# Optimization experiments

Measured on AMD Instinct MI355X. Metric: run time of the kernel, lower is better.

## Reference

```python
import jax, jax.numpy as jnp
import numpy as np

ALPHA = 0.2   # LeakyReLU negative slope
NEG = -9e15   # mask fill value from the torch code


def _conv1d(x, w, b):
    # x: (N, C_in, L), w: (C_out, C_in, 5), padding=2 -> same length
    y = jax.lax.conv_general_dilated(x, w, window_strides=(1,), padding=[(2, 2)],
                                     dimension_numbers=('NCH', 'OIH', 'NCH'))
    return y + b[None, :, None]


def _gat(h, mask, W, a):
    # Faithful to a_input @ a: e_ij = leakyrelu(Wh_i . a[:H] + Wh_j . a[H:])
    Wh = jnp.einsum('bnf,fo->bno', h, W)          # (B,N,H)
    H = W.shape[1]
    f1 = Wh @ a[:H]                               # (B,N,1)
    f2 = Wh @ a[H:]                               # (B,N,1)
    e = f1 + jnp.swapaxes(f2, 1, 2)               # (B,N,N)
    e = jnp.where(e > 0, e, ALPHA * e)            # LeakyReLU
    e = jnp.where(mask, e, NEG)
    att = jax.nn.softmax(e, axis=-1)              # dropout skipped (eval mode)
    return jnp.einsum('bij,bjo->bio', att, Wh)


def setup_inputs() -> dict:
    key = jax.random.key(0)
    ks = jax.random.split(key, 14)
    B, S, N, H, E = 8, 200, 512, 64, 2048
    sc = 0.1
    return {
        'x': jax.random.normal(ks[0], (B, S, N * 2), dtype=jnp.float32),
        'adj': jax.random.randint(ks[1], (N, N), 0, 2, dtype=jnp.int32),
        'edge_index': jax.random.randint(ks[2], (E, 2), 0, N, dtype=jnp.int32),
        'conv1_w': jax.random.normal(ks[3], (H // 2, 2, 5), dtype=jnp.float32) * sc,
        'conv1_b': jnp.zeros((H // 2,), dtype=jnp.float32),
        'conv2_w': jax.random.normal(ks[4], (H, H // 2, 5), dtype=jnp.float32) * sc,
        'conv2_b': jnp.zeros((H,), dtype=jnp.float32),
        'W1': jax.random.normal(ks[5], (H, H), dtype=jnp.float32) * sc,
        'a1': jax.random.normal(ks[6], (2 * H, 1), dtype=jnp.float32) * sc,
        'W2': jax.random.normal(ks[7], (H, H), dtype=jnp.float32) * sc,
        'a2': jax.random.normal(ks[8], (2 * H, 1), dtype=jnp.float32) * sc,
        'fc1_w': jax.random.normal(ks[9], (2 * H, H), dtype=jnp.float32) * sc,
        'fc1_b': jnp.zeros((H,), dtype=jnp.float32),
        'fc2_w': jax.random.normal(ks[10], (H, 1), dtype=jnp.float32) * sc,
        'fc2_b': jnp.zeros((1,), dtype=jnp.float32),
    }


def reference(x, adj, edge_index, conv1_w, conv1_b, conv2_w, conv2_b,
              W1, a1, W2, a2, fc1_w, fc1_b, fc2_w, fc2_b):
    B = x.shape[0]
    N = adj.shape[0]
    # (B,S,2N) -> (B,N,S,2) -> (B*N,2,S)
    xn = x.reshape(B, -1, N, 2).transpose(0, 2, 1, 3)
    xf = xn.reshape(B * N, -1, 2).transpose(0, 2, 1)
    h = jax.nn.relu(_conv1d(xf, conv1_w, conv1_b))
    h = jax.nn.relu(_conv1d(h, conv2_w, conv2_b))
    h = h.mean(axis=-1)                 # AdaptiveAvgPool1d(1) + squeeze
    h = h.reshape(B, N, -1)             # (B,N,H)
    mask = (adj > 0)[None]              # (1,N,N) broadcasts over batch
    h = jax.nn.relu(_gat(h, mask, W1, a1))
    h = _gat(h, mask, W2, a2)
    h1 = h[:, edge_index[:, 0]]         # (B,E,H)
    h2 = h[:, edge_index[:, 1]]
    he = jnp.concatenate([h1, h2], axis=-1)  # (B,E,2H)
    z = jax.nn.relu(he @ fc1_w + fc1_b)
    return jax.nn.sigmoid(z @ fc2_w + fc2_b).squeeze(-1)  # (B,E)
```

## Files before the change

kernel.cpp:

```cpp
#include <hip/hip_runtime.h>
#include <hip/hip_bf16.h>

typedef unsigned short u16;
typedef __attribute__((ext_vector_type(8))) short short8;
typedef __attribute__((ext_vector_type(4))) float float4v;

#define BATCH 8
#define SLEN  200
#define NNODE 512
#define NEDGE 2048
#define NEGV  -9000000000000000.0f

#define H1S 40
#define H1R 212

__device__ __forceinline__ u16 f2bf(float f) {
    unsigned int x = __float_as_uint(f);
    unsigned int lsb = (x >> 16) & 1u;
    x += 0x7fffu + lsb;
    return (u16)(x >> 16);
}

__device__ __forceinline__ float bf2f(u16 u) {
    return __uint_as_float(((unsigned int)u) << 16);
}

__device__ __forceinline__ unsigned int pk2(float a, float b) {
    __hip_bfloat162 h = __float22bfloat162_rn(make_float2(a, b));
    unsigned int r;
    __builtin_memcpy(&r, &h, 4);
    return r;
}

__global__ __launch_bounds__(256) void pre_kernel(
    const int* __restrict__ adj,
    const float* __restrict__ w2,
    const float* __restrict__ fc1w,
    const float* __restrict__ W2g,
    u16* __restrict__ w2f,
    u16* __restrict__ efw,
    u16* __restrict__ w2gf,
    u16* __restrict__ msk)
{
    const int t = threadIdx.x;
    const int blk = blockIdx.x;

    if (blk == 0) {
        for (int idx = t; idx < 20 * 64 * 8; idx += 256) {
            const int fid = idx >> 9, rem = idx & 511;
            const int lane = rem >> 3, j = rem & 7;
            const int kk = fid >> 2, ot = fid & 3;
            const int ml = lane & 15, q = lane >> 4;
            const int c  = q * 8 + j;
            const int ic = (c & 1) * 16 + (c >> 1);
            const int oc = ot * 16 + ml;
            w2f[idx] = f2bf(w2[(size_t)oc * 160 + ic * 5 + kk]);
        }
        return;
    }
    if (blk == 1) {
        for (int idx = t; idx < 16 * 64 * 8; idx += 256) {
            const int u = idx >> 9, rem = idx & 511;
            const int lane = rem >> 3, j = rem & 7;
            const int ks = u >> 2, wvv = u & 3;
            const int ml = lane & 15, q = lane >> 4;
            const int o = wvv * 16 + ml;
            const int k = ks * 32 + q * 8 + j;
            efw[idx] = f2bf(fc1w[k * 64 + o]);
        }
        return;
    }
    if (blk == 2) {
        for (int idx = t; idx < 8 * 64 * 8; idx += 256) {
            const int u = idx >> 9, rem = idx & 511;
            const int lane = rem >> 3, j = rem & 7;
            const int kh = u >> 2, nt = u & 3;
            const int ml = lane & 15, q = lane >> 4;
            const int o = nt * 16 + ml;
            const int k = kh * 32 + q * 8 + j;
            w2gf[idx] = f2bf(W2g[k * 64 + o]);
        }
        return;
    }

    {
        const int tid   = (blk - 3) * 256 + t;
        const int row   = tid >> 5;
        const int chunk = tid & 31;
        const int4* ap = (const int4*)(adj + (size_t)row * 512 + chunk * 16);
        const int4 a0 = ap[0], a1 = ap[1], a2 = ap[2], a3 = ap[3];
        unsigned int bits = 0;
        bits |= (a0.x > 0) ? 0x0001u : 0u;  bits |= (a0.y > 0) ? 0x0002u : 0u;
        bits |= (a0.z > 0) ? 0x0004u : 0u;  bits |= (a0.w > 0) ? 0x0008u : 0u;
        bits |= (a1.x > 0) ? 0x0010u : 0u;  bits |= (a1.y > 0) ? 0x0020u : 0u;
        bits |= (a1.z > 0) ? 0x0040u : 0u;  bits |= (a1.w > 0) ? 0x0080u : 0u;
        bits |= (a2.x > 0) ? 0x0100u : 0u;  bits |= (a2.y > 0) ? 0x0200u : 0u;
        bits |= (a2.z > 0) ? 0x0400u : 0u;  bits |= (a2.w > 0) ? 0x0800u : 0u;
        bits |= (a3.x > 0) ? 0x1000u : 0u;  bits |= (a3.y > 0) ? 0x2000u : 0u;
        bits |= (a3.z > 0) ? 0x4000u : 0u;  bits |= (a3.w > 0) ? 0x8000u : 0u;
        msk[row * 32 + chunk] = (u16)bits;
    }
}

__global__ __launch_bounds__(256) void conv_fused_kernel(
    const float* __restrict__ x,
    const float* __restrict__ w1,
    const float* __restrict__ b1,
    const float* __restrict__ b2,
    const float* __restrict__ W1,
    const float* __restrict__ a1,
    const u16* __restrict__ w2f,
    u16* __restrict__ Wh_bt,
    float* __restrict__ f1,
    float* __restrict__ f2)
{
    __shared__ float xs[2][2][212];
    __shared__ __align__(16) u16 h1p[H1R * H1S];
    __shared__ float red[4][2][32];
    __shared__ float hm[2][64];
    __shared__ float part[2][4][64];

    const int t    = threadIdx.x;
    const int blk  = blockIdx.x;
    const int b    = blk >> 8;
    const int pair = blk & 255;
    const int n0   = pair * 2;
    const int lane = t & 63;
    const int wv   = t >> 6;
    const int ml   = lane & 15;
    const int q    = lane >> 4;
    const int p = t & 15;
    const int g = t >> 4;
    const int o2 = wv & 1;
    const int mh = wv >> 1;

    short8 wfA[5], wfB[5];
    #pragma unroll
    for (int kk = 0; kk < 5; ++kk) {
        wfA[kk] = *(const short8*)(w2f + ((kk * 4 + o2 * 2 + 0) * 64 + lane) * 8);
        wfB[kk] = *(const short8*)(w2f + ((kk * 4 + o2 * 2 + 1) * 64 + lane) * 8);
    }
    const float bias2a = b2[o2 * 32 + ml];
    const float bias2b = b2[o2 * 32 + 16 + ml];

    float wA[10], wB[10];
    #pragma unroll
    for (int j = 0; j < 10; ++j) {
        wA[j] = w1[p * 10 + j];
        wB[j] = w1[(16 + p) * 10 + j];
    }
    const float b1a = b1[p], b1b = b1[16 + p];

    if (t < SLEN) {
        const float4 xv = *(const float4*)(x + ((size_t)(b * SLEN + t)) * 1024 + 4 * pair);
        xs[0][0][2 + t] = xv.x;
        xs[0][1][2 + t] = xv.y;
        xs[1][0][2 + t] = xv.z;
        xs[1][1][2 + t] = xv.w;
    } else if (t < 212) {
        const int pp = (t < 202) ? (t - 200) : t;
        xs[0][0][pp] = 0.f; xs[0][1][pp] = 0.f;
        xs[1][0][pp] = 0.f; xs[1][1][pp] = 0.f;
    }
    {
        unsigned int* hz = (unsigned int*)h1p;
        if (t < 40)       hz[t] = 0u;
        else if (t < 240) hz[4000 + t] = 0u;
    }
    __syncthreads();

    float tAn[2], tBn[2];
    for (int nd = 0; nd < 2; ++nd) {
        #pragma unroll
        for (int u = 0; u < 4; ++u) {
            const int base = 4 * g + 64 * u;
            if (base < SLEN) {
                float X0[8], X1[8];
                *(float4*)&X0[0] = *(const float4*)&xs[nd][0][base];
                *(float4*)&X0[4] = *(const float4*)&xs[nd][0][base + 4];
                *(float4*)&X1[0] = *(const float4*)&xs[nd][1][base];
                *(float4*)&X1[4] = *(const float4*)&xs[nd][1][base + 4];
                #pragma unroll
                for (int i = 0; i < 4; ++i) {
                    float a0 = b1a, a1v = b1b;
                    #pragma unroll
                    for (int k = 0; k < 5; ++k) {
                        const float x0 = X0[i + k], x1 = X1[i + k];
                        a0  += wA[k] * x0 + wA[5 + k] * x1;
                        a1v += wB[k] * x0 + wB[5 + k] * x1;
                    }
                    *(unsigned int*)&h1p[(2 + base + i) * H1S + 2 * p] =
                        pk2(fmaxf(a0, 0.f), fmaxf(a1v, 0.f));
                }
            }
        }
        __syncthreads();

        float tA = 0.f, tB = 0.f;
        const int mt0 = mh * 7, mtE = mh ? 13 : 7;
        for (int mt = mt0; mt < mtE; ++mt) {
            float4v acc0 = {0.f, 0.f, 0.f, 0.f};
            float4v acc1 = {0.f, 0.f, 0.f, 0.f};
            #pragma unroll
            for (int kk = 0; kk < 5; ++kk) {
                const short8 a = *(const short8*)&h1p[(mt * 16 + ml + kk) * H1S + q * 8];
                acc0 = __builtin_amdgcn_mfma_f32_16x16x32_bf16(a, wfA[kk], acc0, 0, 0, 0);
                acc1 = __builtin_amdgcn_mfma_f32_16x16x32_bf16(a, wfB[kk], acc1, 0, 0, 0);
            }
            if (mt < 12) {
                #pragma unroll
                for (int r = 0; r < 4; ++r) {
                    tA += fmaxf(acc0[r] + bias2a, 0.f);
                    tB += fmaxf(acc1[r] + bias2b, 0.f);
                }
            } else if (q < 2) {
                #pragma unroll
                for (int r = 0; r < 4; ++r) {
                    tA += fmaxf(acc0[r] + bias2a, 0.f);
                    tB += fmaxf(acc1[r] + bias2b, 0.f);
                }
            }
        }
        tA += __shfl_xor(tA, 16, 64);
        tA += __shfl_xor(tA, 32, 64);
        tB += __shfl_xor(tB, 16, 64);
        tB += __shfl_xor(tB, 32, 64);
        tAn[nd] = tA;
        tBn[nd] = tB;
        __syncthreads();
    }

    if (lane < 16) {
        red[wv][0][ml]      = tAn[0];
        red[wv][0][16 + ml] = tBn[0];
        red[wv][1][ml]      = tAn[1];
        red[wv][1][16 + ml] = tBn[1];
    }
    __syncthreads();
    if (t < 128) {
        const int nd = t >> 6, o = t & 63;
        const int grp = (o >> 5), idx = o & 31;
        hm[nd][o] = (red[grp][nd][idx] + red[grp + 2][nd][idx]) * (1.0f / 200.0f);
    }
    __syncthreads();

    {
        const int o = t & 63, q4 = t >> 6;
        const float* Wp = W1 + (q4 * 16) * 64 + o;
        float p0 = 0.f, p1 = 0.f;
        #pragma unroll
        for (int k = 0; k < 16; ++k) {
            const float w = Wp[k * 64];
            p0 += hm[0][q4 * 16 + k] * w;
            p1 += hm[1][q4 * 16 + k] * w;
        }
        part[0][q4][o] = p0;
        part[1][q4][o] = p1;
    }
    __syncthreads();
    if (t < 128) {
        const int nd = t >> 6, o = t & 63;
        const int n = n0 + nd;
        const float v = part[nd][0][o] + part[nd][1][o] + part[nd][2][o] + part[nd][3][o];
        Wh_bt[((size_t)(b * 64 + o)) * 512 + n] = f2bf(v);
        float v1 = v * a1[o];
        float v2 = v * a1[64 + o];
        #pragma unroll
        for (int off = 32; off; off >>= 1) {
            v1 += __shfl_xor(v1, off, 64);
            v2 += __shfl_xor(v2, off, 64);
        }
        if (o == 0) { f1[b * 512 + n] = v1; f2[b * 512 + n] = v2; }
    }
}

#define PSTR 520
__global__ __launch_bounds__(512) void gat_attn_kernel(
    const u16* __restrict__ Wh_bt,
    const float* __restrict__ f1in,
    const float* __restrict__ f2in,
    const u16* __restrict__ msk,
    const u16* __restrict__ w2gf,
    const float* __restrict__ a2,
    u16* __restrict__ whbt_out,
    float* __restrict__ f1out,
    float* __restrict__ f2out,
    float* __restrict__ outp,
    const int fuse)
{
    __shared__ __align__(16) u16 P[16 * PSTR];
    __shared__ float f2s[512];
    __shared__ float invs[16];
    __shared__ float f1s[16];
    __shared__ float accH[4][64][4];
    __shared__ __align__(16) u16 g1s[16 * 72];
    __shared__ __align__(16) u16 wh2s[64 * 20];
    __shared__ float fp1[4][16], fp2[4][16];

    const int t   = threadIdx.x;
    const int blk = blockIdx.x;
    const int b   = blk >> 5;
    const int i0  = (blk & 31) * 16;
    const int lane = t & 63, wv = t >> 6, nt = wv & 3, kh = wv >> 2;
    const int ml = lane & 15, q = lane >> 4;

    const u16* Bp = Wh_bt + ((size_t)(b * 64 + nt * 16 + ml)) * 512 + kh * 256 + q * 8;
    short8 bfr[8];
    #pragma unroll
    for (int ks = 0; ks < 8; ++ks)
        bfr[ks] = *(const short8*)(Bp + ks * 32);

    f2s[t & 511] = f2in[b * 512 + (t & 511)];
    if (t < 16) f1s[t] = f1in[b * 512 + i0 + t];
    __syncthreads();

    {
        const int i = t >> 5, jseg = t & 31;
        const float f1i = f1s[i];
        const unsigned int mbits = msk[(size_t)(i0 + i) * 32 + jseg];
        const float* f2p = f2s + jseg * 16;
        float ev[16];
        float mx = -3.0e38f;
        #pragma unroll
        for (int v = 0; v < 16; ++v) {
            float e = f1i + f2p[v];
            e = e > 0.f ? e : 0.2f * e;
            e = ((mbits >> v) & 1u) ? e : NEGV;
            ev[v] = e;
            mx = fmaxf(mx, e);
        }
        mx = fmaxf(mx, __shfl_xor(mx, 1, 64));
        mx = fmaxf(mx, __shfl_xor(mx, 2, 64));
        mx = fmaxf(mx, __shfl_xor(mx, 4, 64));
        mx = fmaxf(mx, __shfl_xor(mx, 8, 64));
        mx = fmaxf(mx, __shfl_xor(mx, 16, 64));
        float sum = 0.f;
        #pragma unroll
        for (int v = 0; v < 16; ++v) {
            const float ex = __expf(ev[v] - mx);
            ev[v] = ex;
            sum += ex;
        }
        sum += __shfl_xor(sum, 1, 64);
        sum += __shfl_xor(sum, 2, 64);
        sum += __shfl_xor(sum, 4, 64);
        sum += __shfl_xor(sum, 8, 64);
        sum += __shfl_xor(sum, 16, 64);
        if (jseg == 0) invs[i] = 1.0f / sum;
        unsigned int* prow = (unsigned int*)&P[i * PSTR + jseg * 16];
        #pragma unroll
        for (int v = 0; v < 8; ++v)
            prow[v] = pk2(ev[2 * v], ev[2 * v + 1]);
    }
    __syncthreads();

    float4v acc = {0.f, 0.f, 0.f, 0.f};
    #pragma unroll
    for (int ks = 0; ks < 8; ++ks) {
        const short8 afr = *(const short8*)&P[ml * PSTR + kh * 256 + ks * 32 + q * 8];
        acc = __builtin_amdgcn_mfma_f32_16x16x32_bf16(afr, bfr[ks], acc, 0, 0, 0);
    }
    if (kh == 1) {
        #pragma unroll
        for (int r = 0; r < 4; ++r) accH[nt][lane][r] = acc[r];
    }
    __syncthreads();
    if (kh == 0) {
        #pragma unroll
        for (int r = 0; r < 4; ++r) {
            const int i2 = q * 4 + r;
            float val = (acc[r] + accH[nt][lane][r]) * invs[i2];
            if (fuse) {
                val = fmaxf(val, 0.f);
                g1s[i2 * 72 + nt * 16 + ml] = f2bf(val);
            } else {
                outp[((size_t)(b * 512 + i0 + i2)) * 64 + nt * 16 + ml] = val;
            }
        }
    }

    if (!fuse) return;

    __syncthreads();
    const short8 af2 = *(const short8*)&g1s[ml * 72 + kh * 32 + q * 8];
    const short8 bf2v = *(const short8*)(w2gf + ((kh * 4 + nt) * 64 + lane) * 8);
    float4v c2 = {0.f, 0.f, 0.f, 0.f};
    c2 = __builtin_amdgcn_mfma_f32_16x16x32_bf16(af2, bf2v, c2, 0, 0, 0);
    if (kh == 1) {
        #pragma unroll
        for (int r = 0; r < 4; ++r) accH[nt][lane][r] = c2[r];
    }
    __syncthreads();
    if (kh == 0) {
        const int o = nt * 16 + ml;
        const float a2o1 = a2[o], a2o2 = a2[64 + o];
        #pragma unroll
        for (int r = 0; r < 4; ++r) {
            const float wv2 = c2[r] + accH[nt][lane][r];
            wh2s[o * 20 + q * 4 + r] = f2bf(wv2);
            float p1 = wv2 * a2o1, p2 = wv2 * a2o2;
            p1 += __shfl_xor(p1, 1, 64); p2 += __shfl_xor(p2, 1, 64);
            p1 += __shfl_xor(p1, 2, 64); p2 += __shfl_xor(p2, 2, 64);
            p1 += __shfl_xor(p1, 4, 64); p2 += __shfl_xor(p2, 4, 64);
            p1 += __shfl_xor(p1, 8, 64); p2 += __shfl_xor(p2, 8, 64);
            if (ml == 0) {
                fp1[nt][q * 4 + r] = p1;
                fp2[nt][q * 4 + r] = p2;
            }
        }
    }
    __syncthreads();
    if (t < 256) {
        const int o = t >> 2, seg = t & 3;
        *(uint2*)&whbt_out[((size_t)(b * 64 + o)) * 512 + i0 + seg * 4] =
            *(const uint2*)&wh2s[o * 20 + seg * 4];
    }
    if (t < 16) {
        f1out[b * 512 + i0 + t] = fp1[0][t] + fp1[1][t] + fp1[2][t] + fp1[3][t];
        f2out[b * 512 + i0 + t] = fp2[0][t] + fp2[1][t] + fp2[2][t] + fp2[3][t];
    }
}

#define FSTR 136
__global__ __launch_bounds__(256) void edge_mlp_kernel(
    const float* __restrict__ hg,
    const int* __restrict__ eidx,
    const u16* __restrict__ efw,
    const float* __restrict__ fc1b,
    const float* __restrict__ fc2w,
    const float* __restrict__ fc2b,
    float* __restrict__ out)
{
    __shared__ __align__(16) u16 he[16 * FSTR];
    __shared__ float part[16][4];

    const int t   = threadIdx.x;
    const int blk = blockIdx.x;
    const int b   = blk >> 7;
    const int e0  = (blk & 127) * 16;
    const int lane = t & 63, wv = t >> 6, ml = lane & 15, q = lane >> 4;

    short8 bw[4];
    #pragma unroll
    for (int ks = 0; ks < 4; ++ks)
        bw[ks] = *(const short8*)(efw + ((ks * 4 + wv) * 64 + lane) * 8);
    const int o = 16 * wv + ml;
    const float bo = fc1b[o];
    const float wo = fc2w[o];

    {
        const int ep = t >> 4, p = t & 15;
        const int e = e0 + ep;
        const int node = (p < 8) ? eidx[e * 2] : eidx[e * 2 + 1];
        const int c0 = (p & 7) * 8;
        const float* hp = hg + ((size_t)(b * 512 + node)) * 64 + c0;
        const float4 fa = *(const float4*)hp;
        const float4 fb = *(const float4*)(hp + 4);
        unsigned int* dst = (unsigned int*)&he[ep * FSTR + ((p < 8) ? 0 : 64) + c0];
        dst[0] = pk2(fa.x, fa.y);
        dst[1] = pk2(fa.z, fa.w);
        dst[2] = pk2(fb.x, fb.y);
        dst[3] = pk2(fb.z, fb.w);
    }
    __syncthreads();

    float4v acc = {0.f, 0.f, 0.f, 0.f};
    #pragma unroll
    for (int ks = 0; ks < 4; ++ks) {
        const short8 afr = *(const short8*)&he[ml * FSTR + ks * 32 + q * 8];
        acc = __builtin_amdgcn_mfma_f32_16x16x32_bf16(afr, bw[ks], acc, 0, 0, 0);
    }
    #pragma unroll
    for (int r = 0; r < 4; ++r) {
        float z = fmaxf(acc[r] + bo, 0.f) * wo;
        z += __shfl_xor(z, 1, 64);
        z += __shfl_xor(z, 2, 64);
        z += __shfl_xor(z, 4, 64);
        z += __shfl_xor(z, 8, 64);
        if (ml == 0) part[q * 4 + r][wv] = z;
    }
    __syncthreads();
    if (t < 16) {
        const float v = part[t][0] + part[t][1] + part[t][2] + part[t][3] + fc2b[0];
        out[b * 2048 + e0 + t] = 1.0f / (1.0f + __expf(-v));
    }
}

extern "C" void kernel_launch(void* const* d_in, const int* in_sizes, int n_in,
                              void* d_out, int out_size, void* d_ws, size_t ws_size,
                              hipStream_t stream) {
    const float* x    = (const float*)d_in[0];
    const int* adj    = (const int*)d_in[1];
    const int* eidx   = (const int*)d_in[2];
    const float* w1   = (const float*)d_in[3];
    const float* b1   = (const float*)d_in[4];
    const float* w2   = (const float*)d_in[5];
    const float* b2   = (const float*)d_in[6];
    const float* W1   = (const float*)d_in[7];
    const float* a1   = (const float*)d_in[8];
    const float* W2   = (const float*)d_in[9];
    const float* a2   = (const float*)d_in[10];
    const float* fc1w = (const float*)d_in[11];
    const float* fc1b = (const float*)d_in[12];
    const float* fc2w = (const float*)d_in[13];
    const float* fc2b = (const float*)d_in[14];
    float* out = (float*)d_out;

    float* ws = (float*)d_ws;
    const size_t R = (size_t)BATCH * NNODE;
    float* g     = ws;
    float* f1a   = g + R * 64;
    float* f2a   = f1a + R;
    float* f1b   = f2a + R;
    float* f2b   = f1b + R;
    u16*   whbt1 = (u16*)(f2b + R);
    u16*   whbt2 = whbt1 + R * 64;
    u16*   w2f   = whbt2 + R * 64;
    u16*   efw   = w2f + 10240;
    u16*   w2gf  = efw + 8192;
    u16*   msk   = w2gf + 4096;

    pre_kernel<<<dim3(67), dim3(256), 0, stream>>>(
        adj, w2, fc1w, W2, w2f, efw, w2gf, msk);
    conv_fused_kernel<<<dim3(2048), dim3(256), 0, stream>>>(
        x, w1, b1, b2, W1, a1, w2f, whbt1, f1a, f2a);
    gat_attn_kernel<<<dim3(256), dim3(512), 0, stream>>>(
        whbt1, f1a, f2a, msk, w2gf, a2, whbt2, f1b, f2b, g, 1);
    gat_attn_kernel<<<dim3(256), dim3(512), 0, stream>>>(
        whbt2, f1b, f2b, msk, w2gf, a2, whbt2, f1b, f2b, g, 0);
    edge_mlp_kernel<<<dim3(1024), dim3(256), 0, stream>>>(
        g, eidx, efw, fc1b, fc2w, fc2b, out);
}
```

Baseline: 135.1 us.

## Split fused conv kernel into conv1 and conv2 kernels via global bf16 buffer

```diff
diff --git a/kernel.cpp b/kernel.cpp
--- a/kernel.cpp
+++ b/kernel.cpp
@@ -11,8 +11,8 @@
 #define NEDGE 2048
 #define NEGV  -9000000000000000.0f
 
-#define H1S 40
-#define H1R 212
+#define H1GR 212
+#define H1GS 32
 
 __device__ __forceinline__ u16 f2bf(float f) {
     unsigned int x = __float_as_uint(f);
@@ -102,46 +102,21 @@
     }
 }
 
-__global__ __launch_bounds__(256) void conv_fused_kernel(
+__global__ __launch_bounds__(256) void conv1_kernel(
     const float* __restrict__ x,
     const float* __restrict__ w1,
     const float* __restrict__ b1,
-    const float* __restrict__ b2,
-    const float* __restrict__ W1,
-    const float* __restrict__ a1,
-    const u16* __restrict__ w2f,
-    u16* __restrict__ Wh_bt,
-    float* __restrict__ f1,
-    float* __restrict__ f2)
+    u16* __restrict__ h1g)
 {
     __shared__ float xs[2][2][212];
-    __shared__ __align__(16) u16 h1p[H1R * H1S];
-    __shared__ float red[4][2][32];
-    __shared__ float hm[2][64];
-    __shared__ float part[2][4][64];
 
     const int t    = threadIdx.x;
     const int blk  = blockIdx.x;
     const int b    = blk >> 8;
     const int pair = blk & 255;
-    const int n0   = pair * 2;
-    const int lane = t & 63;
-    const int wv   = t >> 6;
-    const int ml   = lane & 15;
-    const int q    = lane >> 4;
     const int p = t & 15;
     const int g = t >> 4;
-    const int o2 = wv & 1;
-    const int mh = wv >> 1;
-
-    short8 wfA[5], wfB[5];
-    #pragma unroll
-    for (int kk = 0; kk < 5; ++kk) {
-        wfA[kk] = *(const short8*)(w2f + ((kk * 4 + o2 * 2 + 0) * 64 + lane) * 8);
-        wfB[kk] = *(const short8*)(w2f + ((kk * 4 + o2 * 2 + 1) * 64 + lane) * 8);
-    }
-    const float bias2a = b2[o2 * 32 + ml];
-    const float bias2b = b2[o2 * 32 + 16 + ml];
+    const int ng0 = b * 512 + pair * 2;
 
     float wA[10], wB[10];
     #pragma unroll
@@ -162,15 +137,22 @@
         xs[0][0][pp] = 0.f; xs[0][1][pp] = 0.f;
         xs[1][0][pp] = 0.f; xs[1][1][pp] = 0.f;
     }
+
     {
-        unsigned int* hz = (unsigned int*)h1p;
-        if (t < 40)       hz[t] = 0u;
-        else if (t < 240) hz[4000 + t] = 0u;
-    }
-    __syncthreads();
-
-    float tAn[2], tBn[2];
+        unsigned int* hg32 = (unsigned int*)h1g;
+        for (int idx = t; idx < 384; idx += 256) {
+            const int nd = (idx >= 192);
+            const int i2 = idx - nd * 192;
+            const int off = (i2 < 32) ? i2 : (202 * 16 + (i2 - 32));
+            hg32[(size_t)(ng0 + nd) * (H1GR * 16) + off] = 0u;
+        }
+    }
+    __syncthreads();
+
+    unsigned int* hg32 = (unsigned int*)h1g;
+    #pragma unroll
     for (int nd = 0; nd < 2; ++nd) {
+        const size_t nbase = (size_t)(ng0 + nd) * (H1GR * 16);
         #pragma unroll
         for (int u = 0; u < 4; ++u) {
             const int base = 4 * g + 64 * u;
@@ -189,88 +171,110 @@
                         a0  += wA[k] * x0 + wA[5 + k] * x1;
                         a1v += wB[k] * x0 + wB[5 + k] * x1;
                     }
-                    *(unsigned int*)&h1p[(2 + base + i) * H1S + 2 * p] =
+                    hg32[nbase + (2 + base + i) * 16 + p] =
                         pk2(fmaxf(a0, 0.f), fmaxf(a1v, 0.f));
                 }
             }
         }
-        __syncthreads();
-
-        float tA = 0.f, tB = 0.f;
-        const int mt0 = mh * 7, mtE = mh ? 13 : 7;
-        for (int mt = mt0; mt < mtE; ++mt) {
-            float4v acc0 = {0.f, 0.f, 0.f, 0.f};
-            float4v acc1 = {0.f, 0.f, 0.f, 0.f};
+    }
+}
+
+__global__ __launch_bounds__(256) void conv2_kernel(
+    const u16* __restrict__ h1g,
+    const float* __restrict__ b2,
+    const float* __restrict__ W1,
+    const float* __restrict__ a1,
+    const u16* __restrict__ w2f,
+    u16* __restrict__ Wh_bt,
+    float* __restrict__ f1,
+    float* __restrict__ f2)
+{
+    __shared__ float red[4][32];
+    __shared__ float hm[64];
+    __shared__ float part[4][64];
+
+    const int t    = threadIdx.x;
+    const int blk  = blockIdx.x;
+    const int b    = blk >> 9;
+    const int n    = blk & 511;
+    const int lane = t & 63;
+    const int wv   = t >> 6;
+    const int ml   = lane & 15;
+    const int q    = lane >> 4;
+    const int o2 = wv & 1;
+    const int mh = wv >> 1;
+
+    short8 wfA[5], wfB[5];
+    #pragma unroll
+    for (int kk = 0; kk < 5; ++kk) {
+        wfA[kk] = *(const short8*)(w2f + ((kk * 4 + o2 * 2 + 0) * 64 + lane) * 8);
+        wfB[kk] = *(const short8*)(w2f + ((kk * 4 + o2 * 2 + 1) * 64 + lane) * 8);
+    }
+    const float bias2a = b2[o2 * 32 + ml];
+    const float bias2b = b2[o2 * 32 + 16 + ml];
+
+    const u16* hb = h1g + (size_t)blk * (H1GR * H1GS);
+
+    float tA = 0.f, tB = 0.f;
+    const int mt0 = mh * 7, mtE = mh ? 13 : 7;
+    for (int mt = mt0; mt < mtE; ++mt) {
+        float4v acc0 = {0.f, 0.f, 0.f, 0.f};
+        float4v acc1 = {0.f, 0.f, 0.f, 0.f};
+        #pragma unroll
+        for (int kk = 0; kk < 5; ++kk) {
+            const short8 a = *(const short8*)(hb + (mt * 16 + ml + kk) * H1GS + q * 8);
+            acc0 = __builtin_amdgcn_mfma_f32_16x16x32_bf16(a, wfA[kk], acc0, 0, 0, 0);
+            acc1 = __builtin_amdgcn_mfma_f32_16x16x32_bf16(a, wfB[kk], acc1, 0, 0, 0);
+        }
+        if (mt < 12) {
             #pragma unroll
-            for (int kk = 0; kk < 5; ++kk) {
-                const short8 a = *(const short8*)&h1p[(mt * 16 + ml + kk) * H1S + q * 8];
-                acc0 = __builtin_amdgcn_mfma_f32_16x16x32_bf16(a, wfA[kk], acc0, 0, 0, 0);
-                acc1 = __builtin_amdgcn_mfma_f32_16x16x32_bf16(a, wfB[kk], acc1, 0, 0, 0);
+            for (int r = 0; r < 4; ++r) {
+                tA += fmaxf(acc0[r] + bias2a, 0.f);
+                tB += fmaxf(acc1[r] + bias2b, 0.f);
             }
-            if (mt < 12) {
-                #pragma unroll
-                for (int r = 0; r < 4; ++r) {
-                    tA += fmaxf(acc0[r] + bias2a, 0.f);
-                    tB += fmaxf(acc1[r] + bias2b, 0.f);
-                }
-            } else if (q < 2) {
-                #pragma unroll
-                for (int r = 0; r < 4; ++r) {
-                    tA += fmaxf(acc0[r] + bias2a, 0.f);
-                    tB += fmaxf(acc1[r] + bias2b, 0.f);
-                }
+        } else if (q < 2) {
+            #pragma unroll
+            for (int r = 0; r < 4; ++r) {
+                tA += fmaxf(acc0[r] + bias2a, 0.f);
+                tB += fmaxf(acc1[r] + bias2b, 0.f);
             }
         }
-        tA += __shfl_xor(tA, 16, 64);
-        tA += __shfl_xor(tA, 32, 64);
-        tB += __shfl_xor(tB, 16, 64);
-        tB += __shfl_xor(tB, 32, 64);
-        tAn[nd] = tA;
-        tBn[nd] = tB;
-        __syncthreads();
-    }
-
+    }
+    tA += __shfl_xor(tA, 16, 64);
+    tA += __shfl_xor(tA, 32, 64);
+    tB += __shfl_xor(tB, 16, 64);
+    tB += __shfl_xor(tB, 32, 64);
     if (lane < 16) {
-        red[wv][0][ml]      = tAn[0];
-        red[wv][0][16 + ml] = tBn[0];
-        red[wv][1][ml]      = tAn[1];
-        red[wv][1][16 + ml] = tBn[1];
-    }
-    __syncthreads();
-    if (t < 128) {
-        const int nd = t >> 6, o = t & 63;
-        const int grp = (o >> 5), idx = o & 31;
-        hm[nd][o] = (red[grp][nd][idx] + red[grp + 2][nd][idx]) * (1.0f / 200.0f);
+        red[wv][ml]      = tA;
+        red[wv][16 + ml] = tB;
+    }
+    __syncthreads();
+    if (t < 64) {
+        const int grp = t >> 5, idx = t & 31;
+        hm[t] = (red[grp][idx] + red[grp + 2][idx]) * (1.0f / 200.0f);
     }
     __syncthreads();
 
     {
         const int o = t & 63, q4 = t >> 6;
         const float* Wp = W1 + (q4 * 16) * 64 + o;
-        float p0 = 0.f, p1 = 0.f;
-        #pragma unroll
-        for (int k = 0; k < 16; ++k) {
-            const float w = Wp[k * 64];
-            p0 += hm[0][q4 * 16 + k] * w;
-            p1 += hm[1][q4 * 16 + k] * w;
-        }
-        part[0][q4][o] = p0;
-        part[1][q4][o] = p1;
-    }
-    __syncthreads();
-    if (t < 128) {
-        const int nd = t >> 6, o = t & 63;
-        const int n = n0 + nd;
-        const float v = part[nd][0][o] + part[nd][1][o] + part[nd][2][o] + part[nd][3][o];
-        Wh_bt[((size_t)(b * 64 + o)) * 512 + n] = f2bf(v);
-        float v1 = v * a1[o];
-        float v2 = v * a1[64 + o];
+        float pv = 0.f;
+        #pragma unroll
+        for (int k = 0; k < 16; ++k) pv += hm[q4 * 16 + k] * Wp[k * 64];
+        part[q4][o] = pv;
+    }
+    __syncthreads();
+    if (t < 64) {
+        const float v = part[0][t] + part[1][t] + part[2][t] + part[3][t];
+        Wh_bt[((size_t)(b * 64 + t)) * 512 + n] = f2bf(v);
+        float v1 = v * a1[t];
+        float v2 = v * a1[64 + t];
         #pragma unroll
         for (int off = 32; off; off >>= 1) {
             v1 += __shfl_xor(v1, off, 64);
             v2 += __shfl_xor(v2, off, 64);
         }
-        if (o == 0) { f1[b * 512 + n] = v1; f2[b * 512 + n] = v2; }
+        if (t == 0) { f1[b * 512 + n] = v1; f2[b * 512 + n] = v2; }
     }
 }
 
@@ -519,11 +523,13 @@
     u16*   efw   = w2f + 10240;
     u16*   w2gf  = efw + 8192;
     u16*   msk   = w2gf + 4096;
+    u16*   h1g   = msk + 16384;
 
     pre_kernel<<<dim3(67), dim3(256), 0, stream>>>(
         adj, w2, fc1w, W2, w2f, efw, w2gf, msk);
-    conv_fused_kernel<<<dim3(2048), dim3(256), 0, stream>>>(
-        x, w1, b1, b2, W1, a1, w2f, whbt1, f1a, f2a);
+    conv1_kernel<<<dim3(2048), dim3(256), 0, stream>>>(x, w1, b1, h1g);
+    conv2_kernel<<<dim3(4096), dim3(256), 0, stream>>>(
+        h1g, b2, W1, a1, w2f, whbt1, f1a, f2a);
     gat_attn_kernel<<<dim3(256), dim3(512), 0, stream>>>(
         whbt1, f1a, f2a, msk, w2gf, a2, whbt2, f1b, f2b, g, 1);
     gat_attn_kernel<<<dim3(256), dim3(512), 0, stream>>>(
```

Measured after the change: 166.3 us. +23.1%, slower.
